# Kernel optimization log

Hardware: AMD Instinct MI355X
Metric: run time of the kernel (lower is better)

The kernel has to match this reference:

```python
import jax, jax.numpy as jnp
import numpy as np

KERNEL_MUL = 2.0
KERNEL_NUM = 5


def setup_inputs() -> dict:
    key = jax.random.key(0)
    k1, k2 = jax.random.split(key)
    n, d = 4096, 256
    source = jax.random.normal(k1, (n, d), dtype=jnp.float32)
    target = jax.random.normal(k2, (n, d), dtype=jnp.float32) + 0.5  # slight domain shift
    return {"source": source, "target": target}


def _gaussian_kernel_sum(source, target):
    # total: (2n, d)
    total = jnp.concatenate([source, target], axis=0)
    n_samples = total.shape[0]
    # Pairwise squared L2 via x^2 + y^2 - 2xy (same math as the (2n,2n,d) broadcast)
    sq = jnp.sum(total * total, axis=1)  # (2n,)
    l2 = sq[:, None] + sq[None, :] - 2.0 * (total @ total.T)  # (2n, 2n)
    l2 = jnp.maximum(l2, 0.0)
    # bandwidth from detached distances (torch uses L2_distance.data)
    bandwidth = jax.lax.stop_gradient(jnp.sum(l2)) / (n_samples ** 2 - n_samples)
    bandwidth = bandwidth / (KERNEL_MUL ** (KERNEL_NUM // 2))
    # sum of multi-bandwidth RBF kernels
    kernels = jnp.zeros_like(l2)
    for i in range(KERNEL_NUM):
        kernels = kernels + jnp.exp(-l2 / (bandwidth * (KERNEL_MUL ** i)))
    return kernels


def reference(source, target):
    b = source.shape[0]
    kernels = _gaussian_kernel_sum(source, target)
    xx = jnp.mean(kernels[:b, :b])
    yy = jnp.mean(kernels[b:, b:])
    xy = jnp.mean(kernels[:b, b:])
    yx = jnp.mean(kernels[b:, :b])
    return xx + yy - xy - yx
```

## Files before the change

### kernel.cpp

```cpp
#include <hip/hip_runtime.h>

#define N_TOT 8192
#define NB    4096
#define DDIM  256
#define NTILE 64
#define NBLK  (NTILE * (NTILE + 1) / 2)
#define PGRID (NBLK / 2)
#define PREP_BLKS 256

typedef __bf16 bf16x8 __attribute__((ext_vector_type(8)));
typedef float  f32x4  __attribute__((ext_vector_type(4)));
typedef float  f32x2  __attribute__((ext_vector_type(2)));

__device__ inline unsigned short f2bf_rne(float x) {
    unsigned int u = __float_as_uint(x);
    unsigned int r = (u + 0x7fffu + ((u >> 16) & 1u)) >> 16;
    return (unsigned short)r;
}


__global__ __launch_bounds__(128) void prep(const float* __restrict__ src,
                                            const float* __restrict__ tgt,
                                            float* __restrict__ sq,
                                            unsigned short* __restrict__ totp,
                                            float* __restrict__ colp) {
    __shared__ unsigned short pbuf[2][32 * 136];
    __shared__ float cs[2 * 256];
    int t = threadIdx.x, w = t >> 6, lane = t & 63;
    int panel = blockIdx.x * 2 + w;
    int row0  = panel * 16;

    float4 csum = {0.f, 0.f, 0.f, 0.f};
    int ls_base = (lane >> 1) * 136 + (lane & 1) * 4;
    #pragma unroll
    for (int r = 0; r < 16; ++r) {
        int row = row0 + r;
        const float* rp = (row < NB) ? (src + (size_t)row * DDIM)
                                     : (tgt + (size_t)(row - NB) * DDIM);
        float4 v = ((const float4*)rp)[lane];
        ushort4 o;
        o.x = f2bf_rne(v.x); o.y = f2bf_rne(v.y);
        o.z = f2bf_rne(v.z); o.w = f2bf_rne(v.w);
        *(ushort4*)&pbuf[w][ls_base + r * 8] = o;
        float s = v.x*v.x + v.y*v.y + v.z*v.z + v.w*v.w;
        #pragma unroll
        for (int off = 32; off > 0; off >>= 1) s += __shfl_down(s, off);
        if (lane == 0) sq[row] = s;
        csum.x += v.x; csum.y += v.y; csum.z += v.z; csum.w += v.w;
    }
    #pragma unroll
    for (int it = 0; it < 16; ++it) {
        int g  = it * 256 + lane * 4;
        int kq = g >> 7, wi = g & 127;
        ushort4 o = *(const ushort4*)&pbuf[w][kq * 136 + wi];
        *(ushort4*)(totp + (size_t)panel * 4096 + g) = o;
    }
    cs[w * 256 + lane * 4 + 0] = csum.x;
    cs[w * 256 + lane * 4 + 1] = csum.y;
    cs[w * 256 + lane * 4 + 2] = csum.z;
    cs[w * 256 + lane * 4 + 3] = csum.w;
    __syncthreads();
    colp[blockIdx.x * 256 + t]       = cs[t] + cs[256 + t];
    colp[blockIdx.x * 256 + t + 128] = cs[t + 128] + cs[256 + t + 128];
}

__global__ void finalize_bw(const float* __restrict__ colp,
                            const float* __restrict__ sq,
                            float* __restrict__ wsf) {
    __shared__ float redA[4], redB[4];
    int t = threadIdx.x, lane = t & 63, w = t >> 6;
    float a[8];
    #pragma unroll
    for (int u = 0; u < 8; ++u) a[u] = 0.f;
    for (int b = 0; b < PREP_BLKS; b += 8) {
        #pragma unroll
        for (int u = 0; u < 8; ++u) a[u] += colp[(b + u) * 256 + t];
    }
    float sv = ((a[0] + a[1]) + (a[2] + a[3])) + ((a[4] + a[5]) + (a[6] + a[7]));
    float s8[8];
    #pragma unroll
    for (int u = 0; u < 8; ++u) s8[u] = 0.f;
    for (int i = 0; i < 32; i += 8) {
        #pragma unroll
        for (int u = 0; u < 8; ++u) s8[u] += sq[(i + u) * 256 + t];
    }
    float s1 = ((s8[0] + s8[1]) + (s8[2] + s8[3])) + ((s8[4] + s8[5]) + (s8[6] + s8[7]));
    float v2 = sv * sv;
    #pragma unroll
    for (int off = 32; off > 0; off >>= 1) {
        s1 += __shfl_down(s1, off);
        v2 += __shfl_down(v2, off);
    }
    if (lane == 0) { redA[w] = s1; redB[w] = v2; }
    __syncthreads();
    if (t == 0) {
        float S1   = redA[0] + redA[1] + redA[2] + redA[3];
        float sdot = redB[0] + redB[1] + redB[2] + redB[3];
        float bw_sum = 2.0f * (float)N_TOT * S1 - 2.0f * sdot;
        double denom = (double)N_TOT * (double)N_TOT - (double)N_TOT;
        float bandwidth = (float)((double)bw_sum / denom) * 0.25f;
        wsf[2] = (1.0f / bandwidth) * 0.0625f * 1.44269504f;
    }
}

__global__ __launch_bounds__(256) void mmd_tiles(const unsigned short* __restrict__ totp,
                                                 const float* __restrict__ sq,
                                                 const float* __restrict__ wsf,
                                                 float* __restrict__ part) {
    __shared__ float redf[4];

    int t = threadIdx.x;
    int wid = t >> 6, lane = t & 63;
    int rl = lane & 15, q = lane >> 4;
    float c  = wsf[2];
    float tc = 2.0f * c;

    #pragma unroll 1
    for (int r = 0; r < 2; ++r) {
        int idx = blockIdx.x + r * PGRID;

        int ti = (int)((129.0f - sqrtf(16641.0f - 8.0f * (float)idx)) * 0.5f);
        if (ti > 63) ti = 63;
        if (ti < 0)  ti = 0;
        while ((ti * (129 - ti)) / 2 > idx) --ti;
        while (((ti + 1) * (128 - ti)) / 2 <= idx) ++ti;
        int tj = ti + idx - (ti * (129 - ti)) / 2;

        int gi0 = ti * 128, gj0 = tj * 128;
        int ia = (wid >> 1) * 64, jb = (wid & 1) * 64;

        f32x4 sqi4[4];
        float sqjv[4];
        #pragma unroll
        for (int m = 0; m < 4; ++m)
            sqi4[m] = *(const f32x4*)(sq + gi0 + ia + m * 16 + q * 4);
        #pragma unroll
        for (int n = 0; n < 4; ++n)
            sqjv[n] = sq[gj0 + jb + n * 16 + rl];

        const unsigned short* pa[4];
        const unsigned short* pb[4];
        int pA0 = (gi0 + ia) >> 4, pB0 = (gj0 + jb) >> 4;
        #pragma unroll
        for (int m = 0; m < 4; ++m) {
            pa[m] = totp + (size_t)(pA0 + m) * 4096 + lane * 8;
            pb[m] = totp + (size_t)(pB0 + m) * 4096 + lane * 8;
        }

        f32x4 acc[4][4];
        #pragma unroll
        for (int m = 0; m < 4; ++m)
            #pragma unroll
            for (int n = 0; n < 4; ++n) acc[m][n] = (f32x4){0.f, 0.f, 0.f, 0.f};

        bf16x8 av[2][4], bv[2][4];
        #pragma unroll
        for (int m = 0; m < 4; ++m) {
            av[0][m] = *(const bf16x8*)(pa[m]);
            bv[0][m] = *(const bf16x8*)(pb[m]);
        }
        #pragma unroll
        for (int s = 0; s < 8; ++s) {
            const int cur = s & 1, nxt = cur ^ 1;
            if (s < 7) {
                const int so = (s + 1) * 512;
                #pragma unroll
                for (int m = 0; m < 4; ++m) {
                    av[nxt][m] = *(const bf16x8*)(pa[m] + so);
                    bv[nxt][m] = *(const bf16x8*)(pb[m] + so);
                }
            }
            #pragma unroll
            for (int m = 0; m < 4; ++m)
                #pragma unroll
                for (int n = 0; n < 4; ++n)
                    acc[m][n] = __builtin_amdgcn_mfma_f32_16x16x32_bf16(av[cur][m], bv[cur][n], acc[m][n], 0, 0, 0);
        }

        f32x2 lsum = {0.f, 0.f};
        #pragma unroll
        for (int m = 0; m < 4; ++m) {
            f32x4 ai;
            ai[0] = sqi4[m][0] * c; ai[1] = sqi4[m][1] * c;
            ai[2] = sqi4[m][2] * c; ai[3] = sqi4[m][3] * c;
            #pragma unroll
            for (int n = 0; n < 4; ++n) {
                float bj = sqjv[n] * c;
                #pragma unroll
                for (int ep = 0; ep < 2; ++ep) {
                    f32x2 x;
                    x[0] = __builtin_fmaf(acc[m][n][2*ep+0], tc, -(ai[2*ep+0] + bj));
                    x[1] = __builtin_fmaf(acc[m][n][2*ep+1], tc, -(ai[2*ep+1] + bj));
                    f32x2 E;
                    E[0] = __builtin_amdgcn_exp2f(x[0]);
                    E[1] = __builtin_amdgcn_exp2f(x[1]);
                    f32x2 E2 = E * E, E4 = E2 * E2, E8 = E4 * E4;
                    lsum += ((E + E2) + (E4 + E8)) + E8 * E8;
                }
            }
        }
        float local = lsum[0] + lsum[1];
        #pragma unroll
        for (int off = 32; off > 0; off >>= 1) local += __shfl_down(local, off);
        if (lane == 0) redf[wid] = local;
        __syncthreads();
        if (t == 0) {
            float tot = redf[0] + redf[1] + redf[2] + redf[3];
            float scale = (((ti < 32) == (tj < 32)) ? 1.0f : -1.0f) * ((ti == tj) ? 1.0f : 2.0f);
            part[idx] = tot * scale;
        }
        __syncthreads();
    }
}

__global__ void write_out(const float* __restrict__ part, float* __restrict__ out) {
    __shared__ float red[4];
    int t = threadIdx.x, lane = t & 63, w = t >> 6;
    float s = 0.f;
    for (int i = t; i < NBLK; i += 256) s += part[i];
    #pragma unroll
    for (int off = 32; off > 0; off >>= 1) s += __shfl_down(s, off);
    if (lane == 0) red[w] = s;
    __syncthreads();
    if (t == 0)
        out[0] = (red[0] + red[1] + red[2] + red[3]) * (1.0f / ((float)NB * (float)NB));
}

extern "C" void kernel_launch(void* const* d_in, const int* in_sizes, int n_in,
                              void* d_out, int out_size, void* d_ws, size_t ws_size,
                              hipStream_t stream) {
    const float* src = (const float*)d_in[0];
    const float* tgt = (const float*)d_in[1];
    float* wsf  = (float*)d_ws;
    float* sq   = wsf + 512;
    float* part = wsf + 16384;
    float* colp = wsf + 32768;
    unsigned short* totp = (unsigned short*)((char*)d_ws + 524288);

    prep<<<PREP_BLKS, 128, 0, stream>>>(src, tgt, sq, totp, colp);
    finalize_bw<<<1, 256, 0, stream>>>(colp, sq, wsf);
    mmd_tiles<<<PGRID, 256, 0, stream>>>(totp, sq, wsf, part);
    write_out<<<1, 256, 0, stream>>>(part, (float*)d_out);
}
```

Before: 114.4 us.

## Fold bandwidth finalize into tile kernel via atomics and use persistent grid

Removes the separate single-block finalize kernel: prep now atomically accumulates column sums into a zeroed vector, and every mmd_tiles block redundantly recomputes the bandwidth constant from sq and the column sums. The tile grid changes from 1040 blocks doing two tiles each to 512 blocks looping up to five tiles, with launch bounds requesting two blocks per SM. This cuts one launch and its serialization, but adds a memset, atomic contention, redundant per-block reductions and tail imbalance, since the last block round is only partly filled.

```diff
diff --git a/kernel.cpp b/kernel.cpp
--- a/kernel.cpp
+++ b/kernel.cpp
@@ -5,7 +5,7 @@
 #define DDIM  256
 #define NTILE 64
 #define NBLK  (NTILE * (NTILE + 1) / 2)
-#define PGRID (NBLK / 2)
+#define MGRID 512
 #define PREP_BLKS 256
 
 typedef __bf16 bf16x8 __attribute__((ext_vector_type(8)));
@@ -23,7 +23,7 @@
                                             const float* __restrict__ tgt,
                                             float* __restrict__ sq,
                                             unsigned short* __restrict__ totp,
-                                            float* __restrict__ colp) {
+                                            float* __restrict__ svec) {
     __shared__ unsigned short pbuf[2][32 * 136];
     __shared__ float cs[2 * 256];
     int t = threadIdx.x, w = t >> 6, lane = t & 63;
@@ -60,38 +60,31 @@
     cs[w * 256 + lane * 4 + 2] = csum.z;
     cs[w * 256 + lane * 4 + 3] = csum.w;
     __syncthreads();
-    colp[blockIdx.x * 256 + t]       = cs[t] + cs[256 + t];
-    colp[blockIdx.x * 256 + t + 128] = cs[t + 128] + cs[256 + t + 128];
-}
-
-__global__ void finalize_bw(const float* __restrict__ colp,
-                            const float* __restrict__ sq,
-                            float* __restrict__ wsf) {
-    __shared__ float redA[4], redB[4];
-    int t = threadIdx.x, lane = t & 63, w = t >> 6;
-    float a[8];
-    #pragma unroll
-    for (int u = 0; u < 8; ++u) a[u] = 0.f;
-    for (int b = 0; b < PREP_BLKS; b += 8) {
-        #pragma unroll
-        for (int u = 0; u < 8; ++u) a[u] += colp[(b + u) * 256 + t];
-    }
-    float sv = ((a[0] + a[1]) + (a[2] + a[3])) + ((a[4] + a[5]) + (a[6] + a[7]));
-    float s8[8];
-    #pragma unroll
-    for (int u = 0; u < 8; ++u) s8[u] = 0.f;
-    for (int i = 0; i < 32; i += 8) {
-        #pragma unroll
-        for (int u = 0; u < 8; ++u) s8[u] += sq[(i + u) * 256 + t];
-    }
-    float s1 = ((s8[0] + s8[1]) + (s8[2] + s8[3])) + ((s8[4] + s8[5]) + (s8[6] + s8[7]));
+    atomicAdd(&svec[t],       cs[t] + cs[256 + t]);
+    atomicAdd(&svec[t + 128], cs[t + 128] + cs[256 + t + 128]);
+}
+
+__global__ __launch_bounds__(256, 2) void mmd_tiles(const unsigned short* __restrict__ totp,
+                                                    const float* __restrict__ sq,
+                                                    const float* __restrict__ svec,
+                                                    float* __restrict__ part) {
+    __shared__ float redf[4], redA[4], redB[4], cshare;
+
+    int t = threadIdx.x;
+    int wid = t >> 6, lane = t & 63;
+    int rl = lane & 15, q = lane >> 4;
+
+    float s1 = 0.f;
+    #pragma unroll
+    for (int i = 0; i < 32; ++i) s1 += sq[i * 256 + t];
+    float sv = svec[t];
     float v2 = sv * sv;
     #pragma unroll
     for (int off = 32; off > 0; off >>= 1) {
         s1 += __shfl_down(s1, off);
         v2 += __shfl_down(v2, off);
     }
-    if (lane == 0) { redA[w] = s1; redB[w] = v2; }
+    if (lane == 0) { redA[wid] = s1; redB[wid] = v2; }
     __syncthreads();
     if (t == 0) {
         float S1   = redA[0] + redA[1] + redA[2] + redA[3];
@@ -99,25 +92,16 @@
         float bw_sum = 2.0f * (float)N_TOT * S1 - 2.0f * sdot;
         double denom = (double)N_TOT * (double)N_TOT - (double)N_TOT;
         float bandwidth = (float)((double)bw_sum / denom) * 0.25f;
-        wsf[2] = (1.0f / bandwidth) * 0.0625f * 1.44269504f;
-    }
-}
-
-__global__ __launch_bounds__(256) void mmd_tiles(const unsigned short* __restrict__ totp,
-                                                 const float* __restrict__ sq,
-                                                 const float* __restrict__ wsf,
-                                                 float* __restrict__ part) {
-    __shared__ float redf[4];
-
-    int t = threadIdx.x;
-    int wid = t >> 6, lane = t & 63;
-    int rl = lane & 15, q = lane >> 4;
-    float c  = wsf[2];
+        cshare = (1.0f / bandwidth) * 0.0625f * 1.44269504f;
+    }
+    __syncthreads();
+    float c  = cshare;
     float tc = 2.0f * c;
 
     #pragma unroll 1
-    for (int r = 0; r < 2; ++r) {
-        int idx = blockIdx.x + r * PGRID;
+    for (int r = 0; r < 5; ++r) {
+        int idx = blockIdx.x + r * MGRID;
+        if (idx >= NBLK) break;
 
         int ti = (int)((129.0f - sqrtf(16641.0f - 8.0f * (float)idx)) * 0.5f);
         if (ti > 63) ti = 63;
@@ -232,13 +216,13 @@
     const float* src = (const float*)d_in[0];
     const float* tgt = (const float*)d_in[1];
     float* wsf  = (float*)d_ws;
+    float* svec = wsf + 64;
     float* sq   = wsf + 512;
     float* part = wsf + 16384;
-    float* colp = wsf + 32768;
     unsigned short* totp = (unsigned short*)((char*)d_ws + 524288);
 
-    prep<<<PREP_BLKS, 128, 0, stream>>>(src, tgt, sq, totp, colp);
-    finalize_bw<<<1, 256, 0, stream>>>(colp, sq, wsf);
-    mmd_tiles<<<PGRID, 256, 0, stream>>>(totp, sq, wsf, part);
+    hipMemsetAsync((char*)d_ws + 256, 0, 1024, stream);
+    prep<<<PREP_BLKS, 128, 0, stream>>>(src, tgt, sq, totp, svec);
+    mmd_tiles<<<MGRID, 256, 0, stream>>>(totp, sq, svec, part);
     write_out<<<1, 256, 0, stream>>>(part, (float*)d_out);
 }
```

Result: slower. 118.0 us (+3.1%).
